# Performance work log

Measured on AMD Instinct MI355X. Metric: run time of the kernel, lower is better.

## Reference

```python
import jax, jax.numpy as jnp
import numpy as np

STRIDES = (4, 8, 16, 32)
MAP = 7              # roi_map_size
SR = 2               # sampling ratio
G = MAP * SR         # 14x14 sample grid per RoI
NC = 80              # foreground classes (background class is LAST: bckg_class_first=False)
IMG = 800.0          # canvas size (all images 800x800)
SCORE_THR = 0.05
IOU_THR = 0.5
IMTOP = 100
MIN_SIZE = 0.01
K_NMS = 1000         # pre-NMS top-k kept (jit-friendly stand-in for torch.nonzero filtering)
N_IMG = 2
BBOX_MULTS = (0.1, 0.2)
DWH_CLAMP = float(np.log(1000.0 / 16.0))
OFF = 1000.0         # per (image,class) coordinate offset for batched NMS


def _roi_align_level(fm, boxes, imidx, stride):
    # fm: [B,C,H,W]; boxes: [N,4] xyxy in image coords; returns [N,C,7,7]
    x1, y1, x2, y2 = [boxes[:, i] / stride for i in range(4)]
    H, W = fm.shape[2], fm.shape[3]
    f = (jnp.arange(G, dtype=boxes.dtype) + 0.5) / G
    gx = jnp.clip(x1[:, None] + f[None, :] * (x2 - x1)[:, None], 0.0, W - 1)  # [N,G]
    gy = jnp.clip(y1[:, None] + f[None, :] * (y2 - y1)[:, None], 0.0, H - 1)
    x0 = jnp.floor(gx); y0 = jnp.floor(gy)
    x0i = x0.astype(jnp.int32); y0i = y0.astype(jnp.int32)
    x1i = jnp.minimum(x0i + 1, W - 1); y1i = jnp.minimum(y0i + 1, H - 1)
    lx = gx - x0; ly = gy - y0
    fmt = jnp.transpose(fm, (0, 2, 3, 1))  # [B,H,W,C]
    b = imidx[:, None, None]
    def g(yi, xi):  # -> [N,G,G,C]
        return fmt[b, yi[:, :, None], xi[:, None, :]]
    wy0 = (1 - ly)[:, :, None, None]; wy1 = ly[:, :, None, None]
    wx0 = (1 - lx)[:, None, :, None]; wx1 = lx[:, None, :, None]
    v = (g(y0i, x0i) * (wy0 * wx0) + g(y0i, x1i) * (wy0 * wx1)
         + g(y1i, x0i) * (wy1 * wx0) + g(y1i, x1i) * (wy1 * wx1))
    N, C = boxes.shape[0], fm.shape[1]
    v = v.reshape(N, MAP, SR, MAP, SR, C).mean(axis=(2, 4))  # avg-pool -> [N,7,7,C]
    return jnp.transpose(v, (0, 3, 1, 2))  # [N,C,7,7]


def _roi_align_multilevel(boxes, imidx, fmaps):
    w = boxes[:, 2] - boxes[:, 0]
    h = boxes[:, 3] - boxes[:, 1]
    lvl = jnp.floor(4.0 + jnp.log2(jnp.sqrt(jnp.maximum(w * h, 1e-6)) / 224.0))
    lvl = jnp.clip(lvl, 2.0, 5.0).astype(jnp.int32) - 2  # FPN level index 0..3
    out = 0.0
    for l, (fm, s) in enumerate(zip(fmaps, STRIDES)):
        v = _roi_align_level(fm, boxes, imidx, float(s))
        out = out + jnp.where((lvl == l)[:, None, None, None], v, 0.0)
    return out


def _iou_matrix(b):
    area = (b[:, 2] - b[:, 0]) * (b[:, 3] - b[:, 1])
    lt = jnp.maximum(b[:, None, :2], b[None, :, :2])
    rb = jnp.minimum(b[:, None, 2:], b[None, :, 2:])
    wh = jnp.clip(rb - lt, 0.0)
    inter = wh[..., 0] * wh[..., 1]
    return inter / jnp.maximum(area[:, None] + area[None, :] - inter, 1e-9)


def _forward(proposals, imidx, fm0, fm1, fm2, fm3,
             W_fc0, b_fc0, W_fc1, b_fc1, W_cls, b_cls, W_reg, b_reg):
    N = proposals.shape[0]
    roi = _roi_align_multilevel(proposals, imidx, (fm0, fm1, fm2, fm3))  # [N,C,7,7]
    x = roi.reshape(N, -1)
    x = jax.nn.relu(x @ W_fc0 + b_fc0)
    x = jax.nn.relu(x @ W_fc1 + b_fc1)
    reg = (x @ W_reg + b_reg).reshape(N, NC, 4)
    log = x @ W_cls + b_cls                      # [N, NC+1]
    scr = jax.nn.softmax(log, axis=-1)[:, :-1]   # drop background (last)
    # proposals -> cxcywh
    pw = proposals[:, 2] - proposals[:, 0]
    ph = proposals[:, 3] - proposals[:, 1]
    pcx = proposals[:, 0] + 0.5 * pw
    pcy = proposals[:, 1] + 0.5 * ph
    mx, mw = BBOX_MULTS
    dx = reg[..., 0] * mx; dy = reg[..., 1] * mx
    dw = jnp.minimum(reg[..., 2] * mw, DWH_CLAMP)
    dh = jnp.minimum(reg[..., 3] * mw, DWH_CLAMP)
    cx = pcx[:, None] + dx * pw[:, None]
    cy = pcy[:, None] + dy * ph[:, None]
    bw = pw[:, None] * jnp.exp(dw)
    bh = ph[:, None] * jnp.exp(dh)
    x1 = jnp.clip(cx - 0.5 * bw, 0.0, IMG)
    y1 = jnp.clip(cy - 0.5 * bh, 0.0, IMG)
    x2 = jnp.clip(cx + 0.5 * bw, 0.0, IMG)
    y2 = jnp.clip(cy + 0.5 * bh, 0.0, IMG)
    boxes = jnp.stack([x1, y1, x2, y2], axis=-1).reshape(N * NC, 4)
    scores = scr.reshape(N * NC)
    cls = jnp.tile(jnp.arange(NC, dtype=jnp.int32), (N,))
    iix = jnp.repeat(imidx.astype(jnp.int32), NC)
    valid = (scores > SCORE_THR) \
        & ((x2 - x1).reshape(-1) >= MIN_SIZE) & ((y2 - y1).reshape(-1) >= MIN_SIZE)
    ms = jnp.where(valid, scores, -1.0)
    top_s, top_i = jax.lax.top_k(ms, K_NMS)      # sorted descending
    b_k = boxes[top_i]; c_k = cls[top_i]; i_k = iix[top_i]
    off = (i_k * NC + c_k).astype(boxes.dtype) * OFF
    iou = _iou_matrix(b_k + off[:, None])        # class/image-offset batched NMS
    keep0 = top_s > 0.0
    idxs = jnp.arange(K_NMS)
    def body(i, keep):
        sup = (iou[i] > IOU_THR) & keep[i] & (idxs > i)
        return keep & (~sup)
    keep = jax.lax.fori_loop(0, K_NMS, body, keep0)
    bs, ss, cs = [], [], []
    for im in range(N_IMG):
        si = jnp.where(keep & (i_k == im), top_s, -1.0)
        v, j = jax.lax.top_k(si, IMTOP)
        ok = v > 0.0
        bs.append(jnp.where(ok[:, None], b_k[j], 0.0))
        ss.append(jnp.where(ok, v, 0.0))
        cs.append(jnp.where(ok, c_k[j], -1))
    return jnp.stack(bs), jnp.stack(ss), jnp.stack(cs)


def setup_inputs() -> dict:
    key = jax.random.key(0)
    ks = jax.random.split(key, 16)
    B, N, C = 2, 1000, 256
    cx = jax.random.uniform(ks[0], (N,), minval=50.0, maxval=750.0)
    cy = jax.random.uniform(ks[1], (N,), minval=50.0, maxval=750.0)
    bw = jax.random.uniform(ks[2], (N,), minval=16.0, maxval=320.0)
    bh = jax.random.uniform(ks[3], (N,), minval=16.0, maxval=320.0)
    proposals = jnp.stack([jnp.clip(cx - bw / 2, 0.0, 800.0), jnp.clip(cy - bh / 2, 0.0, 800.0),
                           jnp.clip(cx + bw / 2, 0.0, 800.0), jnp.clip(cy + bh / 2, 0.0, 800.0)], axis=-1)
    imidx = jax.random.randint(ks[4], (N,), 0, B, dtype=jnp.int32)
    fm0 = jax.random.normal(ks[5], (B, C, 200, 200), jnp.float32)
    fm1 = jax.random.normal(ks[6], (B, C, 100, 100), jnp.float32)
    fm2 = jax.random.normal(ks[7], (B, C, 50, 50), jnp.float32)
    fm3 = jax.random.normal(ks[8], (B, C, 25, 25), jnp.float32)
    clin, c1 = 1024, C * MAP * MAP
    W_fc0 = jax.random.normal(ks[9], (c1, clin), jnp.float32) * 0.01
    b_fc0 = jnp.zeros((clin,), jnp.float32)
    W_fc1 = jax.random.normal(ks[10], (clin, clin), jnp.float32) * 0.02
    b_fc1 = jnp.zeros((clin,), jnp.float32)
    W_cls = jax.random.normal(ks[11], (clin, NC + 1), jnp.float32) * 0.05
    b_cls = jnp.zeros((NC + 1,), jnp.float32)
    W_reg = jax.random.normal(ks[12], (clin, NC * 4), jnp.float32) * 0.02
    b_reg = jnp.zeros((NC * 4,), jnp.float32)
    return {"proposals": proposals, "imidx": imidx, "fm0": fm0, "fm1": fm1, "fm2": fm2, "fm3": fm3,
            "W_fc0": W_fc0, "b_fc0": b_fc0, "W_fc1": W_fc1, "b_fc1": b_fc1,
            "W_cls": W_cls, "b_cls": b_cls, "W_reg": W_reg, "b_reg": b_reg}


def reference(proposals, imidx, fm0, fm1, fm2, fm3,
              W_fc0, b_fc0, W_fc1, b_fc1, W_cls, b_cls, W_reg, b_reg):
    return _forward(proposals, imidx, fm0, fm1, fm2, fm3,
                    W_fc0, b_fc0, W_fc1, b_fc1, W_cls, b_cls, W_reg, b_reg)
```

## Files before the change

kernel.cpp:

```cpp
#include <hip/hip_runtime.h>
#include <hip/hip_bf16.h>
#include <stdint.h>
#include <stddef.h>

typedef __hip_bfloat16 bf16;
typedef short bf16x8s __attribute__((ext_vector_type(8)));
typedef float f32x4 __attribute__((ext_vector_type(4)));
typedef unsigned long long u64;

#define NPROP 1000
#define MPAD  1024
#define NCG   80
#define NCLS  81
#define CH    256
#define KDIM  12544
#define KPAD  12800
#define CLIN  1024
#define NHEAD 512
#define IMGSZ 800.0f
#define SCORE_THR 0.05f
#define MIN_SIZE 0.01f
#define KNMS 1000
#define CAND 4096
#define DWH_CLAMP_F 4.135166556742356f

__device__ __forceinline__ void async_load16(const void* g, void* l) {
    __builtin_amdgcn_global_load_lds(
        (const __attribute__((address_space(1))) void*)g,
        (__attribute__((address_space(3))) void*)l, 16, 0, 0);
}

__device__ __forceinline__ unsigned short bfbits(float x) {
    return __builtin_bit_cast(unsigned short, __float2bfloat16(x));
}

__device__ __forceinline__ void tile64(const float* __restrict__ src, size_t cstride,
                                       int sBase, int sMax,
                                       bf16* __restrict__ dst, size_t ldo) {
    __shared__ unsigned short tile[64][66];
    int tid = threadIdx.x;
    int s4 = (tid & 15) * 4;
    int sg = sBase + s4;
#pragma unroll
    for (int g = 0; g < 4; ++g) {
        int cl = g * 16 + (tid >> 4);
        const float* p = src + (size_t)cl * cstride;
        float4 v = make_float4(0.f, 0.f, 0.f, 0.f);
        if (sg + 3 < sMax) {
            v = *(const float4*)(p + sg);
        } else {
            if (sg + 0 < sMax) v.x = p[sg + 0];
            if (sg + 1 < sMax) v.y = p[sg + 1];
            if (sg + 2 < sMax) v.z = p[sg + 2];
        }
        unsigned lo = (unsigned)bfbits(v.x) | ((unsigned)bfbits(v.y) << 16);
        unsigned hi = (unsigned)bfbits(v.z) | ((unsigned)bfbits(v.w) << 16);
        unsigned* q = (unsigned*)&tile[cl][s4];
        q[0] = lo; q[1] = hi;
    }
    __syncthreads();
    int sl = tid >> 2;
    int cg16 = (tid & 3) * 16;
    if (sBase + sl < sMax) {
        unsigned short r[16];
#pragma unroll
        for (int i = 0; i < 16; ++i) r[i] = tile[cg16 + i][sl];
        uint4 o0, o1;
        o0.x = (unsigned)r[0]  | ((unsigned)r[1]  << 16);
        o0.y = (unsigned)r[2]  | ((unsigned)r[3]  << 16);
        o0.z = (unsigned)r[4]  | ((unsigned)r[5]  << 16);
        o0.w = (unsigned)r[6]  | ((unsigned)r[7]  << 16);
        o1.x = (unsigned)r[8]  | ((unsigned)r[9]  << 16);
        o1.y = (unsigned)r[10] | ((unsigned)r[11] << 16);
        o1.z = (unsigned)r[12] | ((unsigned)r[13] << 16);
        o1.w = (unsigned)r[14] | ((unsigned)r[15] << 16);
        uint4* dp = (uint4*)(dst + (size_t)(sBase + sl) * ldo + cg16);
        dp[0] = o0; dp[1] = o1;
    }
}

__global__ __launch_bounds__(256) void fm_t64(
    const float* __restrict__ f0, const float* __restrict__ f1,
    const float* __restrict__ f2, const float* __restrict__ f3,
    bf16* __restrict__ o0, bf16* __restrict__ o1,
    bf16* __restrict__ o2, bf16* __restrict__ o3) {
    int tx = blockIdx.x;
    int cg = blockIdx.y;
    int b = blockIdx.z;
    const float* fm; bf16* ft; int S;
    if (tx < 625)      { fm = f0; ft = o0; S = 40000; }
    else if (tx < 782) { fm = f1; ft = o1; S = 10000; tx -= 625; }
    else if (tx < 822) { fm = f2; ft = o2; S = 2500;  tx -= 782; }
    else               { fm = f3; ft = o3; S = 625;   tx -= 822; }
    const float* src = fm + ((size_t)b * CH + cg * 64) * S;
    bf16* dst = ft + (size_t)b * S * CH + cg * 64;
    tile64(src, (size_t)S, tx * 64, S, dst, CH);
}

__global__ __launch_bounds__(256) void wfc0_t64(const float* __restrict__ W, bf16* __restrict__ Wt) {
    int tn = blockIdx.x;
    int cg = blockIdx.y;
    int cell = blockIdx.z;
    const float* src = W + (size_t)cell * CLIN + (size_t)(cg * 64) * 50176;
    bf16* dst = Wt + cell * 256 + cg * 64;
    tile64(src, 50176, tn * 64, 1024, dst, KPAD);
}

__global__ void wt0_zero(bf16* __restrict__ Wt) {
    int i = blockIdx.x * 256 + threadIdx.x;
    int n = i >> 7, c2 = i & 127;
    ((unsigned*)Wt)[(size_t)n * (KPAD / 2) + 49 * 128 + c2] = 0u;
}

__global__ void wsmall(const float* __restrict__ Wfc1,
                       const float* __restrict__ Wc, const float* __restrict__ Wr,
                       bf16* __restrict__ Wt1, bf16* __restrict__ Wth) {
    __shared__ float tile[32][33];
    int kBase = blockIdx.x * 32;
    int yy = blockIdx.y;
    int tx = threadIdx.x, ty = threadIdx.y;
    if (yy < 32) {
        int nBase = yy * 32;
#pragma unroll
        for (int i = 0; i < 4; ++i) {
            int k = kBase + ty + i * 8;
            tile[ty + i * 8][tx] = Wfc1[(size_t)k * CLIN + nBase + tx];
        }
        __syncthreads();
#pragma unroll
        for (int i = 0; i < 4; ++i) {
            int n = nBase + ty + i * 8;
            Wt1[(size_t)n * CLIN + kBase + tx] = __float2bfloat16(tile[tx][ty + i * 8]);
        }
    } else {
        int jBase = (yy - 32) * 32;
#pragma unroll
        for (int i = 0; i < 4; ++i) {
            int k = kBase + ty + i * 8;
            int j = jBase + tx;
            float v = 0.f;
            if (j < NCLS) v = Wc[(size_t)k * NCLS + j];
            else if (j >= 128 && j < 448) v = Wr[(size_t)k * (NCG * 4) + (j - 128)];
            tile[ty + i * 8][tx] = v;
        }
        __syncthreads();
#pragma unroll
        for (int i = 0; i < 4; ++i) {
            int j = jBase + ty + i * 8;
            Wth[(size_t)j * CLIN + kBase + tx] = __float2bfloat16(tile[tx][ty + i * 8]);
        }
    }
}

__global__ __launch_bounds__(256) void roi_align(
    const float* __restrict__ props, const int* __restrict__ imidx,
    const bf16* __restrict__ f0, const bf16* __restrict__ f1,
    const bf16* __restrict__ f2, const bf16* __restrict__ f3,
    bf16* __restrict__ x0) {
    int n = blockIdx.x;
    int t = threadIdx.x;
    unsigned* outp = (unsigned*)(x0 + (size_t)n * KPAD);
    if (n >= NPROP) {
        for (int i = t; i < KPAD / 2; i += 256) outp[i] = 0u;
        return;
    }
    __shared__ int4  soff[196];
    __shared__ float4 swt[196];
    float px1 = props[n * 4 + 0], py1 = props[n * 4 + 1];
    float px2 = props[n * 4 + 2], py2 = props[n * 4 + 3];
    float w = px2 - px1, h = py2 - py1;
    float lvlf = floorf(4.0f + log2f(sqrtf(fmaxf(w * h, 1e-6f)) / 224.0f));
    int lvl = (int)fminf(fmaxf(lvlf, 2.0f), 5.0f) - 2;
    const bf16* fmt; int H, Wd; float inv;
    if (lvl == 0)      { fmt = f0; H = 200; Wd = 200; inv = 0.25f; }
    else if (lvl == 1) { fmt = f1; H = 100; Wd = 100; inv = 0.125f; }
    else if (lvl == 2) { fmt = f2; H = 50;  Wd = 50;  inv = 0.0625f; }
    else               { fmt = f3; H = 25;  Wd = 25;  inv = 0.03125f; }
    const unsigned* basep = (const unsigned*)(fmt + (size_t)imidx[n] * H * Wd * CH);
    if (t < 196) {
        int py = t / 14, px = t - py * 14;
        float x1s = px1 * inv, y1s = py1 * inv;
        float dxs = w * inv, dys = h * inv;
        float fx = ((float)px + 0.5f) * (1.0f / 14.0f);
        float fy = ((float)py + 0.5f) * (1.0f / 14.0f);
        float gx = fminf(fmaxf(x1s + fx * dxs, 0.f), (float)(Wd - 1));
        float gy = fminf(fmaxf(y1s + fy * dys, 0.f), (float)(H - 1));
        float x0f = floorf(gx), y0f = floorf(gy);
        int x0i = (int)x0f, y0i = (int)y0f;
        int x1i = min(x0i + 1, Wd - 1), y1i = min(y0i + 1, H - 1);
        float lx = gx - x0f, ly = gy - y0f;
        int4 so;
        so.x = (y0i * Wd + x0i) * (CH / 2);
        so.y = (y0i * Wd + x1i) * (CH / 2);
        so.z = (y1i * Wd + x0i) * (CH / 2);
        so.w = (y1i * Wd + x1i) * (CH / 2);
        soff[t] = so;
        float4 wt;
        wt.x = 0.25f * (1.f - ly) * (1.f - lx);
        wt.y = 0.25f * (1.f - ly) * lx;
        wt.z = 0.25f * ly * (1.f - lx);
        wt.w = 0.25f * ly * lx;
        swt[t] = wt;
    }
    __syncthreads();
    int half = t >> 7;
    int tc = t & 127;
    int c0 = half ? 25 : 0;
    int cN = half ? 24 : 25;
    for (int k = 0; k < cN; ++k) {
        int cell = c0 + k;
        int ci = cell / 7, cj = cell - ci * 7;
        float accL = 0.f, accH = 0.f;
#pragma unroll
        for (int sy = 0; sy < 2; ++sy) {
#pragma unroll
            for (int sx = 0; sx < 2; ++sx) {
                int p = (ci * 2 + sy) * 14 + (cj * 2 + sx);
                int4 so = soff[p];
                float4 wt = swt[p];
                unsigned u;
                u = basep[so.x + tc];
                accL += wt.x * __uint_as_float(u << 16);
                accH += wt.x * __uint_as_float(u & 0xFFFF0000u);
                u = basep[so.y + tc];
                accL += wt.y * __uint_as_float(u << 16);
                accH += wt.y * __uint_as_float(u & 0xFFFF0000u);
                u = basep[so.z + tc];
                accL += wt.z * __uint_as_float(u << 16);
                accH += wt.z * __uint_as_float(u & 0xFFFF0000u);
                u = basep[so.w + tc];
                accL += wt.w * __uint_as_float(u << 16);
                accH += wt.w * __uint_as_float(u & 0xFFFF0000u);
            }
        }
        unsigned lo = (unsigned)bfbits(accL);
        unsigned hi = (unsigned)bfbits(accH);
        outp[cell * 128 + tc] = lo | (hi << 16);
    }
    if (half == 0) outp[49 * 128 + tc] = 0u;
}

#define BM 128
#define BK 64
__global__ __launch_bounds__(256) void gemm_nt(
    const bf16* __restrict__ A, const bf16* __restrict__ B,
    int lda, int kSteps, float* __restrict__ part, int ldc, size_t zStride) {
    __shared__ short Al[BM * BK];
    __shared__ short Bl[BM * BK];
    int tid = threadIdx.x;
    int bmIdx = blockIdx.x;
    int bm = bmIdx * BM;
    int bn = blockIdx.y * BM;
    int nz = gridDim.z;
    int chunk = ((int)blockIdx.z + bmIdx) & (nz - 1);
    int wave = tid >> 6, lane = tid & 63;
    int wm = (wave >> 1) * 64, wn = (wave & 1) * 64;
    int lr = lane & 15, lk = lane >> 4;
    int rowS = wave * 8 + (lane >> 3);
    int colS = (lane & 7) * 8;
    int colSrc = (((lane & 7) ^ ((lane >> 3) & 7))) * 8;

    f32x4 acc[4][4];
#pragma unroll
    for (int i = 0; i < 4; ++i)
#pragma unroll
        for (int j = 0; j < 4; ++j) acc[i][j] = (f32x4){0.f, 0.f, 0.f, 0.f};

    const bf16* gA = A + (size_t)(bm + rowS) * lda + colSrc + (size_t)chunk * kSteps * BK;
    const bf16* gB = B + (size_t)(bn + rowS) * lda + colSrc + (size_t)chunk * kSteps * BK;

    for (int kt = 0; kt < kSteps; ++kt) {
        size_t ko = (size_t)kt * BK;
#pragma unroll
        for (int it = 0; it < 4; ++it) {
            async_load16(gA + ko + (size_t)it * 32 * lda, &Al[(it * 32 + rowS) * BK + colS]);
            async_load16(gB + ko + (size_t)it * 32 * lda, &Bl[(it * 32 + rowS) * BK + colS]);
        }
        asm volatile("s_waitcnt vmcnt(0)" ::: "memory");
        __syncthreads();
#pragma unroll
        for (int ks = 0; ks < 2; ++ks) {
            bf16x8s af[4], bfr[4];
#pragma unroll
            for (int i = 0; i < 4; ++i) {
                int row = wm + i * 16 + lr;
                int ch = ((ks * 4 + lk) ^ (lr & 7)) * 8;
                af[i] = *(const bf16x8s*)&Al[row * BK + ch];
            }
#pragma unroll
            for (int j = 0; j < 4; ++j) {
                int row = wn + j * 16 + lr;
                int ch = ((ks * 4 + lk) ^ (lr & 7)) * 8;
                bfr[j] = *(const bf16x8s*)&Bl[row * BK + ch];
            }
#pragma unroll
            for (int i = 0; i < 4; ++i)
#pragma unroll
                for (int j = 0; j < 4; ++j)
                    acc[i][j] = __builtin_amdgcn_mfma_f32_16x16x32_bf16(af[i], bfr[j], acc[i][j], 0, 0, 0);
        }
        __syncthreads();
    }
    float* outp = part + (size_t)blockIdx.z * zStride;
#pragma unroll
    for (int i = 0; i < 4; ++i) {
        int mbase = bm + wm + i * 16 + lk * 4;
#pragma unroll
        for (int j = 0; j < 4; ++j) {
            int ncol = bn + wn + j * 16 + lr;
#pragma unroll
            for (int r = 0; r < 4; ++r)
                outp[(size_t)(mbase + r) * ldc + ncol] = acc[i][j][r];
        }
    }
}

__global__ void reduceK(const float* __restrict__ part, int nsplit, size_t zStride,
                        const float* __restrict__ bias, int colMask, int relu,
                        bf16* __restrict__ outB, float* __restrict__ outF) {
    int idx = blockIdx.x * 256 + threadIdx.x;
    float v = bias ? bias[idx & colMask] : 0.f;
    for (int s = 0; s < nsplit; ++s) v += part[(size_t)s * zStride + idx];
    if (relu) v = fmaxf(v, 0.f);
    if (outB) outB[idx] = __float2bfloat16(v);
    else outF[idx] = v;
}

__global__ __launch_bounds__(128) void decode(
    const float* __restrict__ heads,
    const float* __restrict__ bcls, const float* __restrict__ breg,
    const float* __restrict__ props, const int* __restrict__ imidx,
    float* __restrict__ boxes, u64* __restrict__ cand, int* __restrict__ cnt) {
    __shared__ float red[128];
    int n = blockIdx.x, t = threadIdx.x;
    float l = (t < NCLS) ? heads[(size_t)n * NHEAD + t] + bcls[t] : -1e30f;
    red[t] = l; __syncthreads();
    for (int s = 64; s > 0; s >>= 1) { if (t < s) red[t] = fmaxf(red[t], red[t + s]); __syncthreads(); }
    float mx = red[0]; __syncthreads();
    float e = (t < NCLS) ? expf(l - mx) : 0.f;
    red[t] = e; __syncthreads();
    for (int s = 64; s > 0; s >>= 1) { if (t < s) red[t] += red[t + s]; __syncthreads(); }
    float denom = red[0];
    if (t >= NCG) return;
    float score = e / denom;
    float px1 = props[n * 4 + 0], py1 = props[n * 4 + 1];
    float px2 = props[n * 4 + 2], py2 = props[n * 4 + 3];
    float pw = px2 - px1, ph = py2 - py1;
    float pcx = px1 + 0.5f * pw, pcy = py1 + 0.5f * ph;
    const float* r4 = heads + (size_t)n * NHEAD + 128 + t * 4;
    float dx = (r4[0] + breg[t * 4 + 0]) * 0.1f;
    float dy = (r4[1] + breg[t * 4 + 1]) * 0.1f;
    float dw = fminf((r4[2] + breg[t * 4 + 2]) * 0.2f, DWH_CLAMP_F);
    float dh = fminf((r4[3] + breg[t * 4 + 3]) * 0.2f, DWH_CLAMP_F);
    float cx = pcx + dx * pw, cy = pcy + dy * ph;
    float bw = pw * expf(dw), bh = ph * expf(dh);
    float x1 = fminf(fmaxf(cx - 0.5f * bw, 0.f), IMGSZ);
    float y1 = fminf(fmaxf(cy - 0.5f * bh, 0.f), IMGSZ);
    float x2 = fminf(fmaxf(cx + 0.5f * bw, 0.f), IMGSZ);
    float y2 = fminf(fmaxf(cy + 0.5f * bh, 0.f), IMGSZ);
    int idx = n * NCG + t;
    float* bo = boxes + (size_t)idx * 4;
    bo[0] = x1; bo[1] = y1; bo[2] = x2; bo[3] = y2;
    bool valid = (score > SCORE_THR) && ((x2 - x1) >= MIN_SIZE) && ((y2 - y1) >= MIN_SIZE);
    if (valid) {
        u64 key = ((u64)__float_as_uint(score) << 17) | (u64)(0x1FFFFu - (unsigned)idx);
        int p = atomicAdd(cnt, 1);
        if (p < CAND) cand[p] = key;
    }
}

__global__ __launch_bounds__(1024) void sort_extract(
    const u64* __restrict__ cand, const int* __restrict__ cntp,
    const float* __restrict__ boxes, const int* __restrict__ imidx,
    float* __restrict__ tb, float* __restrict__ toff,
    float* __restrict__ ts, int* __restrict__ tc, int* __restrict__ ti) {
    __shared__ u64 s[CAND];
    int t = threadIdx.x;
    int n = min(*cntp, CAND);
    if (n > 0) {
        int NS = (n <= 1024) ? 1024 : ((n <= 2048) ? 2048 : 4096);
        int E = NS >> 10;
        for (int p = 0; p < E; ++p) { int i = t + p * 1024; s[i] = (i < n) ? cand[i] : 0ull; }
        __syncthreads();
        for (int k = 2; k <= NS; k <<= 1) {
            for (int j = k >> 1; j > 0; j >>= 1) {
                for (int p = 0; p < E; ++p) {
                    int i = t + p * 1024;
                    int l = i ^ j;
                    if (l > i && l < NS) {
                        u64 a = s[i], b = s[l];
                        bool desc = ((i & k) == 0);
                        if (desc ? (a < b) : (a > b)) { s[i] = b; s[l] = a; }
                    }
                }
                __syncthreads();
            }
        }
    }
    if (t >= KNMS) return;
    u64 key = (n > 0) ? s[t] : 0ull;
    if (key == 0ull) {
        ts[t] = -1.f; tc[t] = -1; ti[t] = -1;
        for (int d = 0; d < 4; ++d) { tb[t * 4 + d] = 0.f; toff[t * 4 + d] = 0.f; }
        return;
    }
    unsigned idx = 0x1FFFFu - (unsigned)(key & 0x1FFFFull);
    float score = __uint_as_float((unsigned)(key >> 17));
    int nn = idx / NCG, c = idx - nn * NCG;
    int im = imidx[nn];
    float off = (float)(im * NCG + c) * 1000.0f;
    for (int d = 0; d < 4; ++d) {
        float v = boxes[(size_t)idx * 4 + d];
        tb[t * 4 + d] = v;
        toff[t * 4 + d] = v + off;
    }
    ts[t] = score; tc[t] = c; ti[t] = im;
}

__global__ __launch_bounds__(256) void nms_write(
    const float* __restrict__ toff, const float* __restrict__ tb,
    const float* __restrict__ ts, const int* __restrict__ tc, const int* __restrict__ ti,
    float* __restrict__ out) {
    __shared__ float4 bx[KNMS];
    __shared__ int kp[KNMS];
    __shared__ int Vsh;
    __shared__ unsigned scan[256];
    int t = threadIdx.x;
    if (t == 0) Vsh = KNMS;
    __syncthreads();
    for (int s = t; s < KNMS; s += 256) {
        bx[s] = ((const float4*)toff)[s];
        bool ok = ts[s] > 0.f;
        kp[s] = ok ? 1 : 0;
        if (!ok) atomicMin(&Vsh, s);
    }
    __syncthreads();
    int V = Vsh;
    for (int i = 0; i < V; ++i) {
        if (kp[i]) {
            float4 bi = bx[i];
            float ai = (bi.z - bi.x) * (bi.w - bi.y);
            for (int j2 = i + 1 + t; j2 < V; j2 += 256) {
                if (!kp[j2]) continue;
                float4 bj = bx[j2];
                float xx1 = fmaxf(bi.x, bj.x), yy1 = fmaxf(bi.y, bj.y);
                float xx2 = fminf(bi.z, bj.z), yy2 = fminf(bi.w, bj.w);
                float iw = fmaxf(xx2 - xx1, 0.f), ih = fmaxf(yy2 - yy1, 0.f);
                float inter = iw * ih;
                float aj = (bj.z - bj.x) * (bj.w - bj.y);
                float iou = inter / fmaxf(ai + aj - inter, 1e-9f);
                if (iou > 0.5f) kp[j2] = 0;
            }
        }
        __syncthreads();
    }
    for (int r = t; r < 200; r += 256) {
        for (int d = 0; d < 4; ++d) out[r * 4 + d] = 0.f;
        out[800 + r] = 0.f;
        out[1000 + r] = -1.0f;
    }
    unsigned loc[4];
    unsigned mycnt = 0;
    #pragma unroll
    for (int q = 0; q < 4; ++q) {
        int s = t * 4 + q;
        unsigned f = 0;
        if (s < KNMS && kp[s] && ts[s] > 0.f) f = (ti[s] == 0) ? 1u : 0x10000u;
        loc[q] = f;
        mycnt += f;
    }
    scan[t] = mycnt;
    __syncthreads();
    for (int d = 1; d < 256; d <<= 1) {
        unsigned v = scan[t];
        unsigned add = (t >= d) ? scan[t - d] : 0u;
        __syncthreads();
        scan[t] = v + add;
        __syncthreads();
    }
    unsigned base = (t > 0) ? scan[t - 1] : 0u;
    #pragma unroll
    for (int q = 0; q < 4; ++q) {
        unsigned f = loc[q];
        if (f) {
            int im = (f >> 16) ? 1 : 0;
            unsigned rank = (im ? (base >> 16) : (base & 0xFFFFu));
            if (rank < 100) {
                int s = t * 4 + q;
                int slot = im * 100 + (int)rank;
                for (int d = 0; d < 4; ++d) out[slot * 4 + d] = tb[s * 4 + d];
                out[800 + slot] = ts[s];
                out[1000 + slot] = (float)tc[s];
            }
            base += f;
        }
    }
}

extern "C" void kernel_launch(void* const* d_in, const int* in_sizes, int n_in,
                              void* d_out, int out_size, void* d_ws, size_t ws_size,
                              hipStream_t stream) {
    (void)in_sizes; (void)n_in; (void)out_size; (void)ws_size;
    const float* props = (const float*)d_in[0];
    const int*   imidx = (const int*)d_in[1];
    const float* fm0 = (const float*)d_in[2];
    const float* fm1 = (const float*)d_in[3];
    const float* fm2 = (const float*)d_in[4];
    const float* fm3 = (const float*)d_in[5];
    const float* Wfc0 = (const float*)d_in[6];
    const float* bfc0 = (const float*)d_in[7];
    const float* Wfc1 = (const float*)d_in[8];
    const float* bfc1 = (const float*)d_in[9];
    const float* Wcls = (const float*)d_in[10];
    const float* bcls = (const float*)d_in[11];
    const float* Wreg = (const float*)d_in[12];
    const float* breg = (const float*)d_in[13];

    char* p = (char*)d_ws;
    auto alloc = [&](size_t bytes) { char* r = p; p += (bytes + 255) & ~(size_t)255; return r; };

    bf16* fmt0 = (bf16*)alloc((size_t)2 * 40000 * CH * 2);
    bf16* fmt1 = (bf16*)alloc((size_t)2 * 10000 * CH * 2);
    bf16* fmt2 = (bf16*)alloc((size_t)2 * 2500 * CH * 2);
    bf16* fmt3 = (bf16*)alloc((size_t)2 * 625 * CH * 2);
    bf16* Wt0 = (bf16*)alloc((size_t)CLIN * KPAD * 2);
    bf16* Wt1 = (bf16*)alloc((size_t)CLIN * CLIN * 2);
    bf16* Wth = (bf16*)alloc((size_t)NHEAD * CLIN * 2);
    bf16* x0 = (bf16*)alloc((size_t)MPAD * KPAD * 2);
    bf16* x1 = (bf16*)alloc((size_t)MPAD * CLIN * 2);
    bf16* x2 = (bf16*)alloc((size_t)MPAD * CLIN * 2);
    float* heads = (float*)alloc((size_t)MPAD * NHEAD * 4);
    float* boxes = (float*)alloc((size_t)NPROP * NCG * 4 * 4);
    u64* cand = (u64*)alloc((size_t)CAND * 8);
    float* tb = (float*)alloc(KNMS * 4 * 4);
    float* toff = (float*)alloc(KNMS * 4 * 4);
    float* ts = (float*)alloc(KNMS * 4);
    int* tc = (int*)alloc(KNMS * 4);
    int* ti = (int*)alloc(KNMS * 4);
    int* cnt = (int*)alloc(256);
    float* Cpart = (float*)fmt0;

    fm_t64<<<dim3(832, 4, 2), 256, 0, stream>>>(fm0, fm1, fm2, fm3, fmt0, fmt1, fmt2, fmt3);
    wfc0_t64<<<dim3(16, 4, 49), 256, 0, stream>>>(Wfc0, Wt0);
    wt0_zero<<<dim3(512), 256, 0, stream>>>(Wt0);
    wsmall<<<dim3(32, 48), dim3(32, 8), 0, stream>>>(Wfc1, Wcls, Wreg, Wt1, Wth);

    roi_align<<<dim3(MPAD), 256, 0, stream>>>(props, imidx, fmt0, fmt1, fmt2, fmt3, x0);

    gemm_nt<<<dim3(8, 8, 8), 256, 0, stream>>>(x0, Wt0, KPAD, 25, Cpart, CLIN, (size_t)MPAD * CLIN);
    reduceK<<<dim3(MPAD * CLIN / 256), 256, 0, stream>>>(Cpart, 8, (size_t)MPAD * CLIN,
        bfc0, CLIN - 1, 1, x1, nullptr);
    gemm_nt<<<dim3(8, 8, 4), 256, 0, stream>>>(x1, Wt1, CLIN, 4, Cpart, CLIN, (size_t)MPAD * CLIN);
    reduceK<<<dim3(MPAD * CLIN / 256), 256, 0, stream>>>(Cpart, 4, (size_t)MPAD * CLIN,
        bfc1, CLIN - 1, 1, x2, nullptr);
    gemm_nt<<<dim3(8, 4, 8), 256, 0, stream>>>(x2, Wth, CLIN, 2, Cpart, NHEAD, (size_t)MPAD * NHEAD);
    reduceK<<<dim3(MPAD * NHEAD / 256), 256, 0, stream>>>(Cpart, 8, (size_t)MPAD * NHEAD,
        nullptr, 0, 0, nullptr, heads);

    hipMemsetAsync(cnt, 0, 4, stream);
    decode<<<dim3(NPROP), 128, 0, stream>>>(heads, bcls, breg, props, imidx, boxes, cand, cnt);
    sort_extract<<<dim3(1), 1024, 0, stream>>>(cand, cnt, boxes, imidx, tb, toff, ts, tc, ti);
    nms_write<<<dim3(1), 256, 0, stream>>>(toff, tb, ts, tc, ti, (float*)d_out);
}
```

Baseline: 197.1 us.

## Gather RoI samples directly from fp32 NCHW maps, dropping feature-map transpose

Removes the kernel that transposed and converted all four FPN feature maps to NHWC bf16 before RoI align. RoI align now reads the fp32 NCHW maps directly: each lane owns one output cell, loops over 64 channels with 16 scattered loads per channel, stages the results in shared memory, then writes packed bf16 rows. This saves a full read and write pass over roughly 27 MB of feature maps. The cost is uncoalesced, strided gathers across channel planes, with only 49 of 64 lanes active. The GEMM partial buffer now gets its own workspace allocation instead of aliasing the removed transpose buffer.

```diff
diff --git a/kernel.cpp b/kernel.cpp
--- a/kernel.cpp
+++ b/kernel.cpp
@@ -79,24 +79,6 @@
     }
 }
 
-__global__ __launch_bounds__(256) void fm_t64(
-    const float* __restrict__ f0, const float* __restrict__ f1,
-    const float* __restrict__ f2, const float* __restrict__ f3,
-    bf16* __restrict__ o0, bf16* __restrict__ o1,
-    bf16* __restrict__ o2, bf16* __restrict__ o3) {
-    int tx = blockIdx.x;
-    int cg = blockIdx.y;
-    int b = blockIdx.z;
-    const float* fm; bf16* ft; int S;
-    if (tx < 625)      { fm = f0; ft = o0; S = 40000; }
-    else if (tx < 782) { fm = f1; ft = o1; S = 10000; tx -= 625; }
-    else if (tx < 822) { fm = f2; ft = o2; S = 2500;  tx -= 782; }
-    else               { fm = f3; ft = o3; S = 625;   tx -= 822; }
-    const float* src = fm + ((size_t)b * CH + cg * 64) * S;
-    bf16* dst = ft + (size_t)b * S * CH + cg * 64;
-    tile64(src, (size_t)S, tx * 64, S, dst, CH);
-}
-
 __global__ __launch_bounds__(256) void wfc0_t64(const float* __restrict__ W, bf16* __restrict__ Wt) {
     int tn = blockIdx.x;
     int cg = blockIdx.y;
@@ -152,31 +134,32 @@
     }
 }
 
-__global__ __launch_bounds__(256) void roi_align(
+__global__ __launch_bounds__(256) void roi_gather(
     const float* __restrict__ props, const int* __restrict__ imidx,
-    const bf16* __restrict__ f0, const bf16* __restrict__ f1,
-    const bf16* __restrict__ f2, const bf16* __restrict__ f3,
+    const float* __restrict__ f0, const float* __restrict__ f1,
+    const float* __restrict__ f2, const float* __restrict__ f3,
     bf16* __restrict__ x0) {
-    int n = blockIdx.x;
-    int t = threadIdx.x;
+    __shared__ int   tabS[16][49];
+    __shared__ float tabW[16][49];
+    __shared__ unsigned short outL[49 * 258];
+    int n = blockIdx.x, t = threadIdx.x;
     unsigned* outp = (unsigned*)(x0 + (size_t)n * KPAD);
     if (n >= NPROP) {
         for (int i = t; i < KPAD / 2; i += 256) outp[i] = 0u;
         return;
     }
-    __shared__ int4  soff[196];
-    __shared__ float4 swt[196];
     float px1 = props[n * 4 + 0], py1 = props[n * 4 + 1];
     float px2 = props[n * 4 + 2], py2 = props[n * 4 + 3];
     float w = px2 - px1, h = py2 - py1;
     float lvlf = floorf(4.0f + log2f(sqrtf(fmaxf(w * h, 1e-6f)) / 224.0f));
     int lvl = (int)fminf(fmaxf(lvlf, 2.0f), 5.0f) - 2;
-    const bf16* fmt; int H, Wd; float inv;
-    if (lvl == 0)      { fmt = f0; H = 200; Wd = 200; inv = 0.25f; }
-    else if (lvl == 1) { fmt = f1; H = 100; Wd = 100; inv = 0.125f; }
-    else if (lvl == 2) { fmt = f2; H = 50;  Wd = 50;  inv = 0.0625f; }
-    else               { fmt = f3; H = 25;  Wd = 25;  inv = 0.03125f; }
-    const unsigned* basep = (const unsigned*)(fmt + (size_t)imidx[n] * H * Wd * CH);
+    const float* fm; int H, Wd; float inv;
+    if (lvl == 0)      { fm = f0; H = 200; Wd = 200; inv = 0.25f; }
+    else if (lvl == 1) { fm = f1; H = 100; Wd = 100; inv = 0.125f; }
+    else if (lvl == 2) { fm = f2; H = 50;  Wd = 50;  inv = 0.0625f; }
+    else               { fm = f3; H = 25;  Wd = 25;  inv = 0.03125f; }
+    int S = H * Wd;
+    const float* base = fm + (size_t)imidx[n] * CH * S;
     if (t < 196) {
         int py = t / 14, px = t - py * 14;
         float x1s = px1 * inv, y1s = py1 * inv;
@@ -189,55 +172,44 @@
         int x0i = (int)x0f, y0i = (int)y0f;
         int x1i = min(x0i + 1, Wd - 1), y1i = min(y0i + 1, H - 1);
         float lx = gx - x0f, ly = gy - y0f;
-        int4 so;
-        so.x = (y0i * Wd + x0i) * (CH / 2);
-        so.y = (y0i * Wd + x1i) * (CH / 2);
-        so.z = (y1i * Wd + x0i) * (CH / 2);
-        so.w = (y1i * Wd + x1i) * (CH / 2);
-        soff[t] = so;
-        float4 wt;
-        wt.x = 0.25f * (1.f - ly) * (1.f - lx);
-        wt.y = 0.25f * (1.f - ly) * lx;
-        wt.z = 0.25f * ly * (1.f - lx);
-        wt.w = 0.25f * ly * lx;
-        swt[t] = wt;
+        int cell = (py >> 1) * 7 + (px >> 1);
+        int sub = (py & 1) * 2 + (px & 1);
+        tabS[sub * 4 + 0][cell] = y0i * Wd + x0i;
+        tabS[sub * 4 + 1][cell] = y0i * Wd + x1i;
+        tabS[sub * 4 + 2][cell] = y1i * Wd + x0i;
+        tabS[sub * 4 + 3][cell] = y1i * Wd + x1i;
+        tabW[sub * 4 + 0][cell] = 0.25f * (1.f - ly) * (1.f - lx);
+        tabW[sub * 4 + 1][cell] = 0.25f * (1.f - ly) * lx;
+        tabW[sub * 4 + 2][cell] = 0.25f * ly * (1.f - lx);
+        tabW[sub * 4 + 3][cell] = 0.25f * ly * lx;
     }
     __syncthreads();
-    int half = t >> 7;
-    int tc = t & 127;
-    int c0 = half ? 25 : 0;
-    int cN = half ? 24 : 25;
-    for (int k = 0; k < cN; ++k) {
-        int cell = c0 + k;
-        int ci = cell / 7, cj = cell - ci * 7;
-        float accL = 0.f, accH = 0.f;
-#pragma unroll
-        for (int sy = 0; sy < 2; ++sy) {
-#pragma unroll
-            for (int sx = 0; sx < 2; ++sx) {
-                int p = (ci * 2 + sy) * 14 + (cj * 2 + sx);
-                int4 so = soff[p];
-                float4 wt = swt[p];
-                unsigned u;
-                u = basep[so.x + tc];
-                accL += wt.x * __uint_as_float(u << 16);
-                accH += wt.x * __uint_as_float(u & 0xFFFF0000u);
-                u = basep[so.y + tc];
-                accL += wt.y * __uint_as_float(u << 16);
-                accH += wt.y * __uint_as_float(u & 0xFFFF0000u);
-                u = basep[so.z + tc];
-                accL += wt.z * __uint_as_float(u << 16);
-                accH += wt.z * __uint_as_float(u & 0xFFFF0000u);
-                u = basep[so.w + tc];
-                accL += wt.w * __uint_as_float(u << 16);
-                accH += wt.w * __uint_as_float(u & 0xFFFF0000u);
-            }
-        }
-        unsigned lo = (unsigned)bfbits(accL);
-        unsigned hi = (unsigned)bfbits(accH);
-        outp[cell * 128 + tc] = lo | (hi << 16);
-    }
-    if (half == 0) outp[49 * 128 + tc] = 0u;
+    int lane = t & 63, wv = t >> 6;
+    if (lane < 49) {
+        int sreg[16]; float wreg[16];
+#pragma unroll
+        for (int k = 0; k < 16; ++k) { sreg[k] = tabS[k][lane]; wreg[k] = tabW[k][lane]; }
+        const float* pc = base + (size_t)wv * 64 * S;
+        unsigned short* orow = &outL[lane * 258 + wv * 64];
+        for (int ci = 0; ci < 64; ++ci) {
+            float acc = 0.f;
+#pragma unroll
+            for (int k = 0; k < 16; ++k) acc += pc[sreg[k]] * wreg[k];
+            orow[ci] = bfbits(acc);
+            pc += S;
+        }
+    }
+    __syncthreads();
+    for (int jj = t; jj < KPAD / 2; jj += 256) {
+        int cell = jj >> 7, i2 = (jj & 127) * 2;
+        unsigned val = 0u;
+        if (cell < 49) {
+            unsigned lo = outL[cell * 258 + i2];
+            unsigned hi = outL[cell * 258 + i2 + 1];
+            val = lo | (hi << 16);
+        }
+        outp[jj] = val;
+    }
 }
 
 #define BM 128
@@ -519,10 +491,7 @@
     char* p = (char*)d_ws;
     auto alloc = [&](size_t bytes) { char* r = p; p += (bytes + 255) & ~(size_t)255; return r; };
 
-    bf16* fmt0 = (bf16*)alloc((size_t)2 * 40000 * CH * 2);
-    bf16* fmt1 = (bf16*)alloc((size_t)2 * 10000 * CH * 2);
-    bf16* fmt2 = (bf16*)alloc((size_t)2 * 2500 * CH * 2);
-    bf16* fmt3 = (bf16*)alloc((size_t)2 * 625 * CH * 2);
+    float* Cpart = (float*)alloc((size_t)8 * MPAD * CLIN * 4);
     bf16* Wt0 = (bf16*)alloc((size_t)CLIN * KPAD * 2);
     bf16* Wt1 = (bf16*)alloc((size_t)CLIN * CLIN * 2);
     bf16* Wth = (bf16*)alloc((size_t)NHEAD * CLIN * 2);
@@ -538,14 +507,12 @@
     int* tc = (int*)alloc(KNMS * 4);
     int* ti = (int*)alloc(KNMS * 4);
     int* cnt = (int*)alloc(256);
-    float* Cpart = (float*)fmt0;
-
-    fm_t64<<<dim3(832, 4, 2), 256, 0, stream>>>(fm0, fm1, fm2, fm3, fmt0, fmt1, fmt2, fmt3);
+
     wfc0_t64<<<dim3(16, 4, 49), 256, 0, stream>>>(Wfc0, Wt0);
     wt0_zero<<<dim3(512), 256, 0, stream>>>(Wt0);
     wsmall<<<dim3(32, 48), dim3(32, 8), 0, stream>>>(Wfc1, Wcls, Wreg, Wt1, Wth);
 
-    roi_align<<<dim3(MPAD), 256, 0, stream>>>(props, imidx, fmt0, fmt1, fmt2, fmt3, x0);
+    roi_gather<<<dim3(MPAD), 256, 0, stream>>>(props, imidx, fm0, fm1, fm2, fm3, x0);
 
     gemm_nt<<<dim3(8, 8, 8), 256, 0, stream>>>(x0, Wt0, KPAD, 25, Cpart, CLIN, (size_t)MPAD * CLIN);
     reduceK<<<dim3(MPAD * CLIN / 256), 256, 0, stream>>>(Cpart, 8, (size_t)MPAD * CLIN,
```

New measurement: 350.8 us. +78.0%, slower.
